# Performance work log

Hardware: AMD Instinct MI355X
Metric: run time of the kernel (lower is better)

Reference implementation:

```python
import jax, jax.numpy as jnp
import numpy as np

K = 32768          # random Fourier features of the integrand
MAX_DEPTH = 4      # fixed unroll depth of the adaptive quadtree


def _f_eval(px, py, w, ax, ay, phi):
    # integrand f(x,y) = sum_k w_k * cos(ax_k x + ay_k y + phi_k)
    theta = px[..., None] * ax + py[..., None] * ay + phi  # (..., K)
    return jnp.cos(theta) @ w


def _simpson_cells(xl, xr, yl, yr, w, ax, ay, phi):
    # 2D Simpson estimate per cell; matches _quad_simpsons2D_mem (center point
    # fp[4] has coefficient 0 in the original formula, so it is skipped).
    mx = (xl + xr) * 0.5
    my = (yl + yr) * 0.5
    px = jnp.stack([xl, mx, xr, xl, xr, xl, mx, xr], axis=-1)  # (N, 8)
    py = jnp.stack([yl, yl, yl, my, my, yr, yr, yr], axis=-1)
    fv = _f_eval(px, py, w, ax, ay, phi)                        # (N, 8)
    hx = jnp.abs(xr - xl)
    hy = jnp.abs(yr - yl)
    return hx * hy / 12.0 * (
        -(fv[..., 0] + fv[..., 2] + fv[..., 5] + fv[..., 7])
        + 4.0 * (fv[..., 1] + fv[..., 3] + fv[..., 4] + fv[..., 6]))


def _split(xl, xr, yl, yr):
    # children in quadrant order q0 (LL), q1 (LR), q2 (UL), q3 (UR), interleaved
    mx = (xl + xr) * 0.5
    my = (yl + yr) * 0.5
    cxl = jnp.stack([xl, mx, xl, mx], -1).reshape(-1)
    cxr = jnp.stack([mx, xr, mx, xr], -1).reshape(-1)
    cyl = jnp.stack([yl, yl, my, my], -1).reshape(-1)
    cyr = jnp.stack([my, my, yr, yr], -1).reshape(-1)
    return cxl, cxr, cyl, cyr


def _adaptive_simpson2d(xa, xb, ya, yb, eps, w, ax, ay, phi):
    xl = jnp.reshape(xa, (1,)); xr = jnp.reshape(xb, (1,))
    yl = jnp.reshape(ya, (1,)); yr = jnp.reshape(yb, (1,))
    bounds = [(xl, xr, yl, yr)]
    S = [_simpson_cells(xl, xr, yl, yr, w, ax, ay, phi)]  # (4**d,) per depth
    wholes = [S[0]]  # 'whole' passed into the asr call for each cell
    for d in range(1, MAX_DEPTH + 1):
        b = _split(*bounds[d - 1])
        bounds.append(b)
        Sd = _simpson_cells(*b, w, ax, ay, phi)
        S.append(Sd)
        W = Sd.reshape(-1, 4)
        # NOTE: original code passes q0 (not q3) as 'whole' for quadrant 3 --
        # this bug is reproduced faithfully.
        wholes.append(jnp.stack([W[:, 0], W[:, 1], W[:, 2], W[:, 0]], -1).reshape(-1))
    val = None
    for d in range(MAX_DEPTH - 1, -1, -1):
        sum_q = S[d + 1].reshape(-1, 4).sum(-1)
        delta = sum_q - wholes[d]
        corrected = sum_q + delta / 15.0
        if d == MAX_DEPTH - 1:
            val = corrected  # truncate recursion at max depth
        else:
            child_sum = val.reshape(-1, 4).sum(-1)
            eps_d = eps / (4.0 ** d)  # eps is quartered at each recursion level
            val = jnp.where(jnp.abs(delta) <= 15.0 * eps_d, corrected, child_sum)
    return val[0]


def setup_inputs() -> dict:
    key = jax.random.key(0)
    k1, k2, k3, k4 = jax.random.split(key, 4)
    w = jax.random.normal(k1, (K,), jnp.float32) / np.float32(np.sqrt(K))
    ax = jax.random.normal(k2, (K,), jnp.float32) * 6.0
    ay = jax.random.normal(k3, (K,), jnp.float32) * 6.0
    phi = jax.random.uniform(k4, (K,), jnp.float32) * np.float32(2.0 * np.pi)
    return {"xa": jnp.float32(0.0), "xb": jnp.float32(1.0),
            "ya": jnp.float32(0.0), "yb": jnp.float32(1.0),
            "eps": jnp.float32(1e-6),
            "w": w, "ax": ax, "ay": ay, "phi": phi}


def reference(xa, xb, ya, yb, eps, w, ax, ay, phi):
    return _adaptive_simpson2d(xa, xb, ya, yb, eps, w, ax, ay, phi)
```

## Files before the change

kernel.cpp:

```cpp
#include <hip/hip_runtime.h>
#include <math.h>

#define KFEAT 32768
#define GRID_N 33
#define NPTS (GRID_N * GRID_N)
#define PTS_PER_BLOCK 8
#define PBLOCKS ((NPTS + PTS_PER_BLOCK - 1) / PTS_PER_BLOCK)
#define SPLITK 16
#define KG 2
#define FP_STRIDE 1092
#define FP_GROUPS (FP_STRIDE / 4)

#define INV2PI 0.15915494309189535f

__device__ __forceinline__ float cos_rev(float rev) {
  float fr, c;
  asm("v_fract_f32 %0, %1" : "=v"(fr) : "v"(rev));
  asm("v_cos_f32 %0, %1" : "=v"(c) : "v"(fr));
  return c;
}

__global__ __launch_bounds__(256) void eval_grid_kernel(
    const float4* __restrict__ w4, const float4* __restrict__ ax4,
    const float4* __restrict__ ay4, const float4* __restrict__ phi4,
    const float* __restrict__ xa_p, const float* __restrict__ xb_p,
    const float* __restrict__ ya_p, const float* __restrict__ yb_p,
    float* __restrict__ Fpart) {
  const int tid = threadIdx.x;
  const int pblk = blockIdx.x;
  const int split = blockIdx.y;
  const float xa = xa_p[0], xb = xb_p[0];
  const float ya = ya_p[0], yb = yb_p[0];
  const float sx = (xb - xa) * (1.0f / 32.0f);
  const float sy = (yb - ya) * (1.0f / 32.0f);

  const int p0 = pblk * PTS_PER_BLOCK;
  float x[PTS_PER_BLOCK], y[PTS_PER_BLOCK];
#pragma unroll
  for (int j = 0; j < PTS_PER_BLOCK; ++j) {
    int p = min(p0 + j, NPTS - 1);
    int gx = p % GRID_N;
    int gy = p / GRID_N;
    x[j] = fmaf((float)gx, sx, xa);
    y[j] = fmaf((float)gy, sy, ya);
  }

  const int base4 = split * ((KFEAT / 4) / SPLITK);
  float4 A[KG], B[KG], P[KG], W[KG];
#pragma unroll
  for (int u = 0; u < KG; ++u) {
    const int idx = base4 + tid + 256 * u;
    A[u] = ax4[idx];
    B[u] = ay4[idx];
    P[u] = phi4[idx];
    W[u] = w4[idx];
  }
#pragma unroll
  for (int u = 0; u < KG; ++u) {
    A[u].x *= INV2PI; A[u].y *= INV2PI; A[u].z *= INV2PI; A[u].w *= INV2PI;
    B[u].x *= INV2PI; B[u].y *= INV2PI; B[u].z *= INV2PI; B[u].w *= INV2PI;
    P[u].x *= INV2PI; P[u].y *= INV2PI; P[u].z *= INV2PI; P[u].w *= INV2PI;
  }

  float acc[PTS_PER_BLOCK];
#pragma unroll
  for (int j = 0; j < PTS_PER_BLOCK; ++j) acc[j] = 0.0f;

#pragma unroll
  for (int u = 0; u < KG; ++u) {
#pragma unroll
    for (int j = 0; j < PTS_PER_BLOCK; ++j) {
      float r0 = fmaf(A[u].x, x[j], fmaf(B[u].x, y[j], P[u].x));
      float r1 = fmaf(A[u].y, x[j], fmaf(B[u].y, y[j], P[u].y));
      float r2 = fmaf(A[u].z, x[j], fmaf(B[u].z, y[j], P[u].z));
      float r3 = fmaf(A[u].w, x[j], fmaf(B[u].w, y[j], P[u].w));
      float s = fmaf(W[u].x, cos_rev(r0), fmaf(W[u].y, cos_rev(r1),
                fmaf(W[u].z, cos_rev(r2), W[u].w * cos_rev(r3))));
      acc[j] += s;
    }
  }

  __shared__ float red[4][PTS_PER_BLOCK];
#pragma unroll
  for (int j = 0; j < PTS_PER_BLOCK; ++j) {
    float v = acc[j];
#pragma unroll
    for (int off = 32; off > 0; off >>= 1) v += __shfl_down(v, off, 64);
    if ((tid & 63) == 0) red[tid >> 6][j] = v;
  }
  __syncthreads();
  if (tid < PTS_PER_BLOCK) {
    const int j = tid;
    float v = red[0][j] + red[1][j] + red[2][j] + red[3][j];
    int p = p0 + j;
    if (p < NPTS) Fpart[split * FP_STRIDE + p] = v;
  }
}

__device__ __forceinline__ int compact_bits(int v, int shift) {
  int r = (v >> shift) & 1;
  r |= ((v >> (shift + 2)) & 1) << 1;
  r |= ((v >> (shift + 4)) & 1) << 2;
  r |= ((v >> (shift + 6)) & 1) << 3;
  return r;
}

__device__ __forceinline__ float simpson_cell(const float* __restrict__ F,
                                              int d, int cell, float hx,
                                              float hy) {
  const int ix = compact_bits(cell, 0);
  const int iy = compact_bits(cell, 1);
  const int s = 5 - d;
  const int h = 1 << (s - 1);
  const int gx0 = ix << s, gx1 = gx0 + h, gx2 = gx0 + 2 * h;
  const int gy0 = iy << s, gy1 = gy0 + h, gy2 = gy0 + 2 * h;
  const float f0 = F[gy0 * GRID_N + gx0];
  const float f1 = F[gy0 * GRID_N + gx1];
  const float f2 = F[gy0 * GRID_N + gx2];
  const float f3 = F[gy1 * GRID_N + gx0];
  const float f4 = F[gy1 * GRID_N + gx2];
  const float f5 = F[gy2 * GRID_N + gx0];
  const float f6 = F[gy2 * GRID_N + gx1];
  const float f7 = F[gy2 * GRID_N + gx2];
  return hx * hy * (1.0f / 12.0f) *
         (-(f0 + f2 + f5 + f7) + 4.0f * (f1 + f3 + f4 + f6));
}

__global__ __launch_bounds__(512) void combine_kernel(
    const float* __restrict__ Fpart, const float* __restrict__ xa_p,
    const float* __restrict__ xb_p, const float* __restrict__ ya_p,
    const float* __restrict__ yb_p, const float* __restrict__ eps_p,
    float* __restrict__ out) {
  __shared__ alignas(16) float Fs[FP_STRIDE];
  __shared__ float S4[256], S3[64], S2[16], S1[4], S0[1];
  __shared__ float val3[64], val2[16], val1[4];
  const int t = threadIdx.x;
  const float xa = *xa_p, xb = *xb_p, ya = *ya_p, yb = *yb_p, eps = *eps_p;
  const float HX = fabsf(xb - xa), HY = fabsf(yb - ya);

  if (t < FP_GROUPS) {
    const float4* Fp4 = (const float4*)Fpart;
    float4 s = make_float4(0.0f, 0.0f, 0.0f, 0.0f);
#pragma unroll
    for (int sp = 0; sp < SPLITK; ++sp) {
      float4 v = Fp4[sp * FP_GROUPS + t];
      s.x += v.x; s.y += v.y; s.z += v.z; s.w += v.w;
    }
    ((float4*)Fs)[t] = s;
  }
  __syncthreads();

  if (t < 256) {
    S4[t] = simpson_cell(Fs, 4, t, HX * 0.0625f, HY * 0.0625f);
    if (t < 64) {
      S3[t] = simpson_cell(Fs, 3, t, HX * 0.125f, HY * 0.125f);
    } else if (t < 80) {
      S2[t - 64] = simpson_cell(Fs, 2, t - 64, HX * 0.25f, HY * 0.25f);
    } else if (t < 84) {
      S1[t - 80] = simpson_cell(Fs, 1, t - 80, HX * 0.5f, HY * 0.5f);
    } else if (t == 84) {
      S0[0] = simpson_cell(Fs, 0, 0, HX, HY);
    }
  }
  __syncthreads();

  if (t < 64) {
    float sumq = ((S4[4 * t] + S4[4 * t + 1]) + S4[4 * t + 2]) + S4[4 * t + 3];
    float whole = ((t & 3) == 3) ? S3[t & ~3] : S3[t];
    float delta = sumq - whole;
    val3[t] = sumq + delta * (1.0f / 15.0f);
  }
  __syncthreads();

  if (t < 16) {
    float sumq = ((S3[4 * t] + S3[4 * t + 1]) + S3[4 * t + 2]) + S3[4 * t + 3];
    float whole = ((t & 3) == 3) ? S2[t & ~3] : S2[t];
    float delta = sumq - whole;
    float corrected = sumq + delta * (1.0f / 15.0f);
    float child =
        ((val3[4 * t] + val3[4 * t + 1]) + val3[4 * t + 2]) + val3[4 * t + 3];
    float eps_d = eps * (1.0f / 16.0f);
    val2[t] = (fabsf(delta) <= 15.0f * eps_d) ? corrected : child;
  }
  __syncthreads();

  if (t < 4) {
    float sumq = ((S2[4 * t] + S2[4 * t + 1]) + S2[4 * t + 2]) + S2[4 * t + 3];
    float whole = ((t & 3) == 3) ? S1[t & ~3] : S1[t];
    float delta = sumq - whole;
    float corrected = sumq + delta * (1.0f / 15.0f);
    float child =
        ((val2[4 * t] + val2[4 * t + 1]) + val2[4 * t + 2]) + val2[4 * t + 3];
    float eps_d = eps * 0.25f;
    val1[t] = (fabsf(delta) <= 15.0f * eps_d) ? corrected : child;
  }
  __syncthreads();

  if (t == 0) {
    float sumq = ((S1[0] + S1[1]) + S1[2]) + S1[3];
    float delta = sumq - S0[0];
    float corrected = sumq + delta * (1.0f / 15.0f);
    float child = ((val1[0] + val1[1]) + val1[2]) + val1[3];
    out[0] = (fabsf(delta) <= 15.0f * eps) ? corrected : child;
  }
}

extern "C" void kernel_launch(void* const* d_in, const int* in_sizes, int n_in,
                              void* d_out, int out_size, void* d_ws,
                              size_t ws_size, hipStream_t stream) {
  const float* xa = (const float*)d_in[0];
  const float* xb = (const float*)d_in[1];
  const float* ya = (const float*)d_in[2];
  const float* yb = (const float*)d_in[3];
  const float* eps = (const float*)d_in[4];
  const float4* w4 = (const float4*)d_in[5];
  const float4* ax4 = (const float4*)d_in[6];
  const float4* ay4 = (const float4*)d_in[7];
  const float4* phi4 = (const float4*)d_in[8];
  float* out = (float*)d_out;
  float* Fpart = (float*)d_ws;

  dim3 grid(PBLOCKS, SPLITK);
  eval_grid_kernel<<<grid, 256, 0, stream>>>(w4, ax4, ay4, phi4, xa, xb, ya,
                                             yb, Fpart);
  combine_kernel<<<1, 512, 0, stream>>>(Fpart, xa, xb, ya, yb, eps, out);
}
```

Baseline: 18.52 us.

## Evaluate only grid points used by Simpson stencils and rebalance split-K

The Simpson stencils never read odd-x points on odd rows of the 33x33 grid, so the eval kernel now computes only the 833 needed points through a compact index map, about a fifth less cosine work. Split-K drops from 16 to 8 with 4 feature groups per thread, which halves the partial sums written and read. The combine kernel runs 1024 threads, reduces the partials in two halves, and scatters the values back into the full grid layout. The cost is a longer per-thread loop and fewer blocks, which lowers the parallelism available to hide latency.

```diff
diff --git a/kernel.cpp b/kernel.cpp
--- a/kernel.cpp
+++ b/kernel.cpp
@@ -4,14 +4,22 @@
 #define KFEAT 32768
 #define GRID_N 33
 #define NPTS (GRID_N * GRID_N)
+#define NQ 833
+#define QSTRIDE 836
+#define QGROUPS (QSTRIDE / 4)
 #define PTS_PER_BLOCK 8
-#define PBLOCKS ((NPTS + PTS_PER_BLOCK - 1) / PTS_PER_BLOCK)
-#define SPLITK 16
-#define KG 2
-#define FP_STRIDE 1092
-#define FP_GROUPS (FP_STRIDE / 4)
+#define PBLOCKS ((NQ + PTS_PER_BLOCK - 1) / PTS_PER_BLOCK)
+#define SPLITK 8
+#define KG 4
 
 #define INV2PI 0.15915494309189535f
+
+__device__ __forceinline__ void q_to_grid(int q, int& gx, int& gy) {
+  int rp = q / 50;
+  int rem = q - 50 * rp;
+  if (rem < 33) { gy = 2 * rp;     gx = rem; }
+  else          { gy = 2 * rp + 1; gx = (rem - 33) * 2; }
+}
 
 __device__ __forceinline__ float cos_rev(float rev) {
   float fr, c;
@@ -38,9 +46,9 @@
   float x[PTS_PER_BLOCK], y[PTS_PER_BLOCK];
 #pragma unroll
   for (int j = 0; j < PTS_PER_BLOCK; ++j) {
-    int p = min(p0 + j, NPTS - 1);
-    int gx = p % GRID_N;
-    int gy = p / GRID_N;
+    int q = min(p0 + j, NQ - 1);
+    int gx, gy;
+    q_to_grid(q, gx, gy);
     x[j] = fmaf((float)gx, sx, xa);
     y[j] = fmaf((float)gy, sy, ya);
   }
@@ -92,8 +100,8 @@
   if (tid < PTS_PER_BLOCK) {
     const int j = tid;
     float v = red[0][j] + red[1][j] + red[2][j] + red[3][j];
-    int p = p0 + j;
-    if (p < NPTS) Fpart[split * FP_STRIDE + p] = v;
+    int q = p0 + j;
+    if (q < NQ) Fpart[split * QSTRIDE + q] = v;
   }
 }
 
@@ -126,27 +134,41 @@
          (-(f0 + f2 + f5 + f7) + 4.0f * (f1 + f3 + f4 + f6));
 }
 
-__global__ __launch_bounds__(512) void combine_kernel(
+__global__ __launch_bounds__(1024) void combine_kernel(
     const float* __restrict__ Fpart, const float* __restrict__ xa_p,
     const float* __restrict__ xb_p, const float* __restrict__ ya_p,
     const float* __restrict__ yb_p, const float* __restrict__ eps_p,
     float* __restrict__ out) {
-  __shared__ alignas(16) float Fs[FP_STRIDE];
+  __shared__ alignas(16) float Fq[2][QSTRIDE];
+  __shared__ float Fs[NPTS];
   __shared__ float S4[256], S3[64], S2[16], S1[4], S0[1];
   __shared__ float val3[64], val2[16], val1[4];
   const int t = threadIdx.x;
   const float xa = *xa_p, xb = *xb_p, ya = *ya_p, yb = *yb_p, eps = *eps_p;
   const float HX = fabsf(xb - xa), HY = fabsf(yb - ya);
 
-  if (t < FP_GROUPS) {
+  if (t < 2 * QGROUPS) {
+    const int quad = (t >= QGROUPS) ? 1 : 0;
+    const int g = t - quad * QGROUPS;
     const float4* Fp4 = (const float4*)Fpart;
     float4 s = make_float4(0.0f, 0.0f, 0.0f, 0.0f);
 #pragma unroll
-    for (int sp = 0; sp < SPLITK; ++sp) {
-      float4 v = Fp4[sp * FP_GROUPS + t];
+    for (int sp = 0; sp < 4; ++sp) {
+      float4 v = Fp4[(quad * 4 + sp) * QGROUPS + g];
       s.x += v.x; s.y += v.y; s.z += v.z; s.w += v.w;
     }
-    ((float4*)Fs)[t] = s;
+    ((float4*)&Fq[quad][0])[g] = s;
+  }
+  __syncthreads();
+
+  if (t < NQ) {
+    float v = Fq[0][t] + Fq[1][t];
+    int gx, gy;
+    int rp = t / 50;
+    int rem = t - 50 * rp;
+    if (rem < 33) { gy = 2 * rp;     gx = rem; }
+    else          { gy = 2 * rp + 1; gx = (rem - 33) * 2; }
+    Fs[gy * GRID_N + gx] = v;
   }
   __syncthreads();
 
@@ -223,5 +245,5 @@
   dim3 grid(PBLOCKS, SPLITK);
   eval_grid_kernel<<<grid, 256, 0, stream>>>(w4, ax4, ay4, phi4, xa, xb, ya,
                                              yb, Fpart);
-  combine_kernel<<<1, 512, 0, stream>>>(Fpart, xa, xb, ya, yb, eps, out);
-}
+  combine_kernel<<<1, 1024, 0, stream>>>(Fpart, xa, xb, ya, yb, eps, out);
+}
```

After: 17.35 us (median of 2 runs). -6.3%, faster.
